# Performance work log

Measured on AMD Instinct MI355X. Metric: run time of the kernel, lower is better.

Reference implementation:

```python
import jax, jax.numpy as jnp
import numpy as np
from jax import lax

BETA = 0.5
IPOT_ITERS = 20


def cosine_cost(x, y):
    # x: [bs, n, D], y: [bs, m, D] -> 1 - cos_sim, [bs, n, m]
    x = x / (jnp.linalg.norm(x, axis=2, keepdims=True) + 1e-12)
    y = y / (jnp.linalg.norm(y, axis=2, keepdims=True) + 1e-12)
    return 1.0 - jnp.einsum('bnd,bmd->bnm', x, y)


def ipot_T(C, miu, nu, beta=BETA, iters=IPOT_ITERS):
    bs, n, m = C.shape
    A = jnp.exp(-C / beta)                    # [bs, n, m]
    sigma0 = jnp.ones((bs, m, 1), C.dtype) / m
    T0 = jnp.ones((bs, n, m), C.dtype)

    def step(carry, _):
        T, sigma = carry
        T = A * T
        delta = miu[:, :, None] / (T @ sigma + 1e-6)            # [bs, n, 1]
        sigma = nu[:, :, None] / (jnp.swapaxes(T, 1, 2) @ delta + 1e-6)  # [bs, m, 1]
        T = delta * T * jnp.swapaxes(sigma, 1, 2)
        return (T, sigma), None

    (T, _), _ = lax.scan(step, (T0, sigma0), None, length=iters)
    return lax.stop_gradient(T)  # original code detaches T


def ipot_distance(C):
    bs, n, m = C.shape
    miu = jnp.ones((bs, n), C.dtype) / n
    nu = jnp.ones((bs, m), C.dtype) / m
    T = ipot_T(C, miu, nu)
    return -jnp.sum(T * C, axis=(1, 2))  # note: original (un-exponentiated) C


def setup_inputs() -> dict:
    key = jax.random.key(0)
    k1, k2, k3, k4 = jax.random.split(key, 4)
    bs, n_sp, n_tm, D = 128, 196, 32, 768
    return {
        'spatial1': jax.random.normal(k1, (bs, n_sp, D), dtype=jnp.float32),
        'spatial2': jax.random.normal(k2, (bs, n_sp, D), dtype=jnp.float32),
        'temporal1': jax.random.normal(k3, (bs, n_tm, D), dtype=jnp.float32),
        'temporal2': jax.random.normal(k4, (bs, n_tm, D), dtype=jnp.float32),
    }


def reference(spatial1, spatial2, temporal1, temporal2):
    C_sp = cosine_cost(spatial1, spatial2)
    C_tm = cosine_cost(temporal1, temporal2)
    spatial_loss = ipot_distance(C_sp)
    temporal_loss = ipot_distance(C_tm)
    return spatial_loss.mean() + temporal_loss.mean()
```

## Files before the change

kernel.cpp:

```cpp
#include <hip/hip_runtime.h>
#include <hip/hip_bf16.h>
#include <cstdint>

typedef float f32x4 __attribute__((ext_vector_type(4)));
typedef __bf16 bf16x8 __attribute__((ext_vector_type(8)));

#define BS 128
#define NSP 196
#define NTM 32
#define DDIM 768

__device__ inline ushort4 f4_to_bf4(float4 v)
{
    ushort4 u;
    u.x = __builtin_bit_cast(unsigned short, (__bf16)v.x);
    u.y = __builtin_bit_cast(unsigned short, (__bf16)v.y);
    u.z = __builtin_bit_cast(unsigned short, (__bf16)v.z);
    u.w = __builtin_bit_cast(unsigned short, (__bf16)v.w);
    return u;
}

__device__ inline bf16x8 f4x2_to_bf8(float4 lo, float4 hi)
{
    bf16x8 r;
    r[0] = (__bf16)lo.x; r[1] = (__bf16)lo.y; r[2] = (__bf16)lo.z; r[3] = (__bf16)lo.w;
    r[4] = (__bf16)hi.x; r[5] = (__bf16)hi.y; r[6] = (__bf16)hi.z; r[7] = (__bf16)hi.w;
    return r;
}

__device__ inline float sumsq4(float4 a)
{
    return fmaf(a.x, a.x, fmaf(a.y, a.y, fmaf(a.z, a.z, a.w * a.w)));
}

__device__ inline float row16_sum(float x)
{
    int t;
    t = __builtin_amdgcn_update_dpp(0, __builtin_bit_cast(int, x), 0x121, 0xf, 0xf, true);
    x += __builtin_bit_cast(float, t);
    t = __builtin_amdgcn_update_dpp(0, __builtin_bit_cast(int, x), 0x122, 0xf, 0xf, true);
    x += __builtin_bit_cast(float, t);
    t = __builtin_amdgcn_update_dpp(0, __builtin_bit_cast(int, x), 0x124, 0xf, 0xf, true);
    x += __builtin_bit_cast(float, t);
    t = __builtin_amdgcn_update_dpp(0, __builtin_bit_cast(int, x), 0x128, 0xf, 0xf, true);
    x += __builtin_bit_cast(float, t);
    return x;
}

__global__ __launch_bounds__(256)
void tm_norm_kernel(const float* __restrict__ tm1, const float* __restrict__ tm2,
                    float* __restrict__ inx_tm, float* __restrict__ iny_tm)
{
    int B = blockIdx.x;
    const float* src; float* inv;
    if (B < 1024) { src = tm1; inv = inx_tm; }
    else          { B -= 1024; src = tm2; inv = iny_tm; }
    const int row  = B * 4 + (threadIdx.x >> 6);
    const int lane = threadIdx.x & 63;
    const float4* p = reinterpret_cast<const float4*>(src + (size_t)row * DDIM);
    float ss = 0.f;
#pragma unroll
    for (int c = 0; c < 3; ++c) ss += sumsq4(p[lane + 64 * c]);
#pragma unroll
    for (int off = 32; off; off >>= 1) ss += __shfl_xor(ss, off, 64);
    if (lane == 0) inv[row] = 1.0f / (sqrtf(ss) + 1e-12f);
}

__global__ __launch_bounds__(448)
void cost_gemm_sp2(const float* __restrict__ X, const float* __restrict__ Y,
                   __bf16* __restrict__ Aout)
{
    __shared__ __bf16 lds[11264];
    float* ldsF = reinterpret_cast<float*>(lds);

    const int flat  = blockIdx.x;
    const int xcd   = flat & 7;
    const int s     = flat >> 3;
    const int b     = xcd * 16 + (s >> 3);
    const int rem   = s & 7;
    const int r0    = (rem >> 2) * 112;
    const int ct_   = rem & 3;
    const int n0    = (ct_ < 3) ? ct_ * 64 : 132;

    const int tid  = threadIdx.x;
    const int w    = tid >> 6, lane = tid & 63;
    const int q    = lane >> 4, l16 = lane & 15;
    const int srow = tid >> 3;
    const int sslt = tid & 7;

    const float* Yb = Y + (size_t)b * NSP * DDIM;

    float4 aL[2], aH[2], bL, bH, b2L, b2H;
    float ssA[2] = {0.f, 0.f};
    float ssB = 0.f, ssB2 = 0.f;

    auto LOADS = [&](int k0) {
#pragma unroll
        for (int p = 0; p < 2; ++p) {
            int gr = b * NSP + r0 + srow + 56 * p;
            gr = min(gr, BS * NSP - 1);
            const float* sp = X + (size_t)gr * DDIM + k0 + sslt * 8;
            aL[p] = *reinterpret_cast<const float4*>(sp);
            aH[p] = *reinterpret_cast<const float4*>(sp + 4);
        }
        {
            const float* sp = Yb + (size_t)(n0 + srow) * DDIM + k0 + sslt * 8;
            bL = *reinterpret_cast<const float4*>(sp);
            bH = *reinterpret_cast<const float4*>(sp + 4);
        }
        if (tid < 64) {
            const float* sp = Yb + (size_t)(n0 + 56 + srow) * DDIM + k0 + sslt * 8;
            b2L = *reinterpret_cast<const float4*>(sp);
            b2H = *reinterpret_cast<const float4*>(sp + 4);
        }
    };
    auto WRITES = [&]() {
#pragma unroll
        for (int p = 0; p < 2; ++p) {
            int r = srow + 56 * p;
            ssA[p] += sumsq4(aL[p]) + sumsq4(aH[p]);
            *reinterpret_cast<bf16x8*>(&lds[r * 64 + ((sslt ^ (r & 7)) << 3)]) =
                f4x2_to_bf8(aL[p], aH[p]);
        }
        {
            int r = srow;
            ssB += sumsq4(bL) + sumsq4(bH);
            *reinterpret_cast<bf16x8*>(&lds[7168 + r * 64 + ((sslt ^ (r & 7)) << 3)]) =
                f4x2_to_bf8(bL, bH);
        }
        if (tid < 64) {
            int r = 56 + srow;
            ssB2 += sumsq4(b2L) + sumsq4(b2H);
            *reinterpret_cast<bf16x8*>(&lds[7168 + r * 64 + ((sslt ^ (r & 7)) << 3)]) =
                f4x2_to_bf8(b2L, b2H);
        }
    };

    f32x4 acc[4];
#pragma unroll
    for (int j = 0; j < 4; ++j) acc[j] = f32x4{0.f, 0.f, 0.f, 0.f};

    LOADS(0);
    for (int kt = 0; kt < 12; ++kt) {
        if (kt) __syncthreads();
        WRITES();
        __syncthreads();
        if (kt < 11) LOADS((kt + 1) * 64);
#pragma unroll
        for (int ks = 0; ks < 2; ++ks) {
            bf16x8 af, bf[4];
            {
                int r = w * 16 + l16;
                af = *reinterpret_cast<const bf16x8*>(
                    &lds[r * 64 + (((ks * 4 + q) ^ (r & 7)) << 3)]);
            }
#pragma unroll
            for (int ct = 0; ct < 4; ++ct) {
                int r = ct * 16 + l16;
                bf[ct] = *reinterpret_cast<const bf16x8*>(
                    &lds[7168 + r * 64 + (((ks * 4 + q) ^ (r & 7)) << 3)]);
            }
#pragma unroll
            for (int ct = 0; ct < 4; ++ct)
                acc[ct] = __builtin_amdgcn_mfma_f32_16x16x32_bf16(af, bf[ct], acc[ct], 0, 0, 0);
        }
    }
    __syncthreads();

#pragma unroll
    for (int p = 0; p < 2; ++p) ldsF[(srow + 56 * p) * 8 + sslt] = ssA[p];
    ldsF[896 + srow * 8 + sslt] = ssB;
    if (tid < 64) ldsF[896 + (56 + srow) * 8 + sslt] = ssB2;
    __syncthreads();

    float ivy[4];
#pragma unroll
    for (int ct = 0; ct < 4; ++ct) {
        int jr = ct * 16 + l16;
        f32x4 s0 = *reinterpret_cast<const f32x4*>(&ldsF[896 + jr * 8]);
        f32x4 s1 = *reinterpret_cast<const f32x4*>(&ldsF[896 + jr * 8 + 4]);
        float ss = (s0.x + s0.y) + (s0.z + s0.w) + (s1.x + s1.y) + (s1.z + s1.w);
        ivy[ct] = 1.0f / (sqrtf(ss) + 1e-12f);
    }
#pragma unroll
    for (int rr = 0; rr < 4; ++rr) {
        int i = w * 16 + q * 4 + rr;
        int gi = r0 + i;
        if (gi < NSP) {
            f32x4 s0 = *reinterpret_cast<const f32x4*>(&ldsF[i * 8]);
            f32x4 s1 = *reinterpret_cast<const f32x4*>(&ldsF[i * 8 + 4]);
            float ss = (s0.x + s0.y) + (s0.z + s0.w) + (s1.x + s1.y) + (s1.z + s1.w);
            float ivx = 1.0f / (sqrtf(ss) + 1e-12f);
#pragma unroll
            for (int ct = 0; ct < 4; ++ct) {
                float cs = acc[ct][rr] * ivx * ivy[ct];
                Aout[(size_t)b * 65536 + (size_t)gi * 256 + (n0 + ct * 16 + l16)] =
                    (__bf16)__expf(2.0f * cs - 2.0f);
            }
        }
    }
}

template<int WROWS, int NWAVES, int BN, int NPTS>
__global__ __launch_bounds__(NWAVES * 64)
void cost_gemm(const float* __restrict__ X, const float* __restrict__ Y,
               const float* __restrict__ invx, const float* __restrict__ invy,
               float* __restrict__ Aout)
{
    constexpr int MT = WROWS * NWAVES;
    constexpr int CT = BN / 16;
    constexpr int RT = WROWS / 16;
    constexpr int KP = 40;
    constexpr int NTH = NWAVES * 64;
    __shared__ __bf16 As[MT][KP];
    __shared__ __bf16 Bs[BN][KP];

    const int b    = blockIdx.y;
    const int row0 = blockIdx.x * MT;
    const int tid  = threadIdx.x;
    const int w    = tid >> 6, lane = tid & 63;
    const int q    = lane >> 4, l16 = lane & 15;
    const float* Xb = X + (size_t)b * NPTS * DDIM;
    const float* Yb = Y + (size_t)b * NPTS * DDIM;

    f32x4 acc[RT][CT];
#pragma unroll
    for (int i = 0; i < RT; ++i)
#pragma unroll
        for (int j = 0; j < CT; ++j) acc[i][j] = f32x4{0.f, 0.f, 0.f, 0.f};

    for (int k0 = 0; k0 < DDIM; k0 += 32) {
        __syncthreads();
        for (int idx = tid * 4; idx < MT * 32; idx += NTH * 4) {
            int r = idx >> 5, kk = idx & 31;
            int gr = row0 + r;
            float4 v = {0.f, 0.f, 0.f, 0.f};
            if (gr < NPTS) v = *reinterpret_cast<const float4*>(Xb + (size_t)gr * DDIM + k0 + kk);
            *reinterpret_cast<ushort4*>(&As[r][kk]) = f4_to_bf4(v);
        }
        for (int idx = tid * 4; idx < BN * 32; idx += NTH * 4) {
            int r = idx >> 5, kk = idx & 31;
            float4 v = {0.f, 0.f, 0.f, 0.f};
            if (r < NPTS) v = *reinterpret_cast<const float4*>(Yb + (size_t)r * DDIM + k0 + kk);
            *reinterpret_cast<ushort4*>(&Bs[r][kk]) = f4_to_bf4(v);
        }
        __syncthreads();

        bf16x8 af[RT];
#pragma unroll
        for (int rt = 0; rt < RT; ++rt)
            af[rt] = *reinterpret_cast<const bf16x8*>(&As[w * WROWS + rt * 16 + l16][q * 8]);
#pragma unroll
        for (int ct = 0; ct < CT; ++ct) {
            bf16x8 bfr = *reinterpret_cast<const bf16x8*>(&Bs[ct * 16 + l16][q * 8]);
#pragma unroll
            for (int rt = 0; rt < RT; ++rt)
                acc[rt][ct] = __builtin_amdgcn_mfma_f32_16x16x32_bf16(af[rt], bfr, acc[rt][ct], 0, 0, 0);
        }
    }

#pragma unroll
    for (int rt = 0; rt < RT; ++rt)
#pragma unroll
        for (int ct = 0; ct < CT; ++ct)
#pragma unroll
            for (int rr = 0; rr < 4; ++rr) {
                int i = row0 + w * WROWS + rt * 16 + q * 4 + rr;
                int j = ct * 16 + l16;
                if (i < NPTS && j < NPTS) {
                    float g  = acc[rt][ct][rr];
                    float cs = g * invx[b * NPTS + i] * invy[b * NPTS + j];
                    Aout[(size_t)b * NPTS * NPTS + (size_t)i * NPTS + j] = expf(-2.0f * (1.0f - cs));
                }
            }
}

__global__ __launch_bounds__(512, 1)
void ipot_dpp(const __bf16* __restrict__ Asp, const float* __restrict__ Atm,
              float* __restrict__ out)
{
    __shared__ __bf16 Alds[224 * 256];
    __shared__ float  cpart[32 * 260];
    __shared__ float  svec[2][272];
    __shared__ float  wsum[8];

    const int B = blockIdx.x;
    if (B >= 128) {
        if (threadIdx.x >= 64) return;
        const int b = B - 128;
        const float* Ab = Atm + (size_t)b * NTM * NTM;
        const int lane = threadIdx.x;
        const int rh = lane >> 5, cj = lane & 31;
        constexpr float MIU = 1.f / NTM;
        float A[16], P[16];
#pragma unroll
        for (int k = 0; k < 16; ++k) {
            A[k] = Ab[(rh + 2 * k) * NTM + cj];
            P[k] = 1.f;
        }
        float sv = MIU;
        for (int it = 0; it < 20; ++it) {
#pragma unroll
            for (int k = 0; k < 16; ++k) {
                P[k] *= A[k];
                float acc = row16_sum(P[k] * sv);
                acc += __shfl_xor(acc, 16);
                P[k] *= MIU * __builtin_amdgcn_rcpf(acc + 1e-6f);
            }
            float cssum = 0.f;
#pragma unroll
            for (int k = 0; k < 16; ++k) cssum += P[k];
            cssum += __shfl_xor(cssum, 32);
            float sg = MIU * __builtin_amdgcn_rcpf(cssum + 1e-6f);
#pragma unroll
            for (int k = 0; k < 16; ++k) P[k] *= sg;
            sv = sg;
        }
        float acc = 0.f;
#pragma unroll
        for (int k = 0; k < 16; ++k)
            acc = fmaf(P[k], -0.5f * __logf(A[k]), acc);
        acc = row16_sum(acc);
        acc += __shfl_xor(acc, 16);
        acc += __shfl_xor(acc, 32);
        if (lane == 0) atomicAdd(out, -acc * (1.f / BS));
        return;
    }

    const int b = (B & 7) * 16 + (B >> 3);
    const __bf16* Ab = Asp + (size_t)b * 65536;
    const int tid = threadIdx.x;
    const int w = tid >> 6, lane = tid & 63;
    const int rq = lane >> 4, cl = lane & 15;
    const int g = w * 4 + rq;
    const int colbase = cl * 8;
    constexpr float MIU = 1.f / NSP;

    for (int idx = tid; idx < NSP * 32; idx += 512) {
        int r = idx >> 5, c = idx & 31;
        bf16x8 v;
#pragma unroll
        for (int i = 0; i < 8; ++i) v[i] = (__bf16)0.f;
        if (c < 25) {
            v = *reinterpret_cast<const bf16x8*>(&Ab[(size_t)r * 256 + c * 8]);
            if (c == 24) { v[4] = (__bf16)0.f; v[5] = (__bf16)0.f; v[6] = (__bf16)0.f; v[7] = (__bf16)0.f; }
        }
        *reinterpret_cast<bf16x8*>(&Alds[r * 256 + c * 8]) = v;
    }
    {
        ushort4 z = {0, 0, 0, 0};
        for (int idx = tid; idx < 28 * 64; idx += 512) {
            int r = 196 + (idx >> 6), c4 = (idx & 63) << 2;
            *reinterpret_cast<ushort4*>(&Alds[r * 256 + c4]) = z;
        }
    }
    __syncthreads();

    float P[7][16];
#pragma unroll
    for (int k = 0; k < 7; ++k)
#pragma unroll
        for (int e = 0; e < 16; ++e) P[k][e] = 1.f;

    float sr[16];
#pragma unroll
    for (int e = 0; e < 16; ++e) {
        int j = (e < 8) ? (colbase + e) : (colbase + 128 + (e - 8));
        sr[e] = (j < NSP) ? MIU : 0.f;
    }

    for (int it = 0; it < 20; ++it) {
        float cs[16];
#pragma unroll
        for (int e = 0; e < 16; ++e) cs[e] = 0.f;

#pragma unroll
        for (int k = 0; k < 7; ++k) {
            const __bf16* ap = &Alds[(g + 32 * k) * 256 + colbase];
            bf16x8 a0 = *reinterpret_cast<const bf16x8*>(ap);
            bf16x8 a1 = *reinterpret_cast<const bf16x8*>(ap + 128);
            float r0 = 0.f, r1 = 0.f;
#pragma unroll
            for (int e = 0; e < 8; ++e) {
                P[k][e] *= (float)a0[e];
                r0 = fmaf(P[k][e], sr[e], r0);
            }
#pragma unroll
            for (int e = 0; e < 8; ++e) {
                P[k][8 + e] *= (float)a1[e];
                r1 = fmaf(P[k][8 + e], sr[8 + e], r1);
            }
            float racc = row16_sum(r0 + r1);
            float delta = MIU * __builtin_amdgcn_rcpf(racc + 1e-6f);
#pragma unroll
            for (int e = 0; e < 16; ++e) {
                P[k][e] *= delta;
                cs[e] += P[k][e];
            }
        }
        {
            float* cp = &cpart[g * 260 + colbase];
            *reinterpret_cast<f32x4*>(cp)     = f32x4{cs[0], cs[1], cs[2], cs[3]};
            *reinterpret_cast<f32x4*>(cp + 4) = f32x4{cs[4], cs[5], cs[6], cs[7]};
            float* cp2 = cp + 128;
            *reinterpret_cast<f32x4*>(cp2)     = f32x4{cs[8], cs[9], cs[10], cs[11]};
            *reinterpret_cast<f32x4*>(cp2 + 4) = f32x4{cs[12], cs[13], cs[14], cs[15]};
        }
        __syncthreads();
        if (tid < 256) {
            float s0 = 0.f, s1 = 0.f, s2 = 0.f, s3 = 0.f;
#pragma unroll
            for (int gg = 0; gg < 32; gg += 4) {
                s0 += cpart[(gg + 0) * 260 + tid];
                s1 += cpart[(gg + 1) * 260 + tid];
                s2 += cpart[(gg + 2) * 260 + tid];
                s3 += cpart[(gg + 3) * 260 + tid];
            }
            float sum = (s0 + s1) + (s2 + s3);
            svec[it & 1][tid] = (tid < NSP) ? (MIU * __builtin_amdgcn_rcpf(sum + 1e-6f)) : 0.f;
        }
        __syncthreads();
        {
            const float* sv = svec[it & 1];
            f32x4 t0 = *reinterpret_cast<const f32x4*>(&sv[colbase]);
            f32x4 t1 = *reinterpret_cast<const f32x4*>(&sv[colbase + 4]);
            f32x4 t2 = *reinterpret_cast<const f32x4*>(&sv[colbase + 128]);
            f32x4 t3 = *reinterpret_cast<const f32x4*>(&sv[colbase + 132]);
            sr[0] = t0.x; sr[1] = t0.y; sr[2] = t0.z; sr[3] = t0.w;
            sr[4] = t1.x; sr[5] = t1.y; sr[6] = t1.z; sr[7] = t1.w;
            sr[8] = t2.x; sr[9] = t2.y; sr[10] = t2.z; sr[11] = t2.w;
            sr[12] = t3.x; sr[13] = t3.y; sr[14] = t3.z; sr[15] = t3.w;
        }
#pragma unroll
        for (int k = 0; k < 7; ++k)
#pragma unroll
            for (int e = 0; e < 16; ++e) P[k][e] *= sr[e];
    }

    float acc = 0.f;
#pragma unroll
    for (int k = 0; k < 7; ++k) {
        const __bf16* ap = &Alds[(g + 32 * k) * 256 + colbase];
        bf16x8 a0 = *reinterpret_cast<const bf16x8*>(ap);
        bf16x8 a1 = *reinterpret_cast<const bf16x8*>(ap + 128);
#pragma unroll
        for (int e = 0; e < 8; ++e) {
            acc = fmaf(P[k][e],     -0.5f * __logf(fmaxf((float)a0[e], 1e-30f)), acc);
            acc = fmaf(P[k][8 + e], -0.5f * __logf(fmaxf((float)a1[e], 1e-30f)), acc);
        }
    }
    acc = row16_sum(acc);
    acc += __shfl_xor(acc, 16);
    acc += __shfl_xor(acc, 32);
    if (lane == 0) wsum[w] = acc;
    __syncthreads();
    if (tid == 0) {
        float t = 0.f;
#pragma unroll
        for (int i = 0; i < 8; ++i) t += wsum[i];
        atomicAdd(out, -t * (1.f / BS));
    }
}

extern "C" void kernel_launch(void* const* d_in, const int* in_sizes, int n_in,
                              void* d_out, int out_size, void* d_ws, size_t ws_size,
                              hipStream_t stream)
{
    const float* sp1 = (const float*)d_in[0];
    const float* sp2 = (const float*)d_in[1];
    const float* tm1 = (const float*)d_in[2];
    const float* tm2 = (const float*)d_in[3];
    float* out = (float*)d_out;
    float* ws  = (float*)d_ws;

    float* inx_tm = ws;
    float* iny_tm = inx_tm + BS * NTM;
    float* A_tm   = iny_tm + BS * NTM;
    __bf16* A_sp  = (__bf16*)(ws + 139264);

    tm_norm_kernel<<<dim3(2048), 256, 0, stream>>>(tm1, tm2, inx_tm, iny_tm);

    cost_gemm_sp2<<<dim3(1024), 448, 0, stream>>>(sp1, sp2, A_sp);

    cost_gemm<16, 2, 32, NTM><<<dim3(1, BS), 128, 0, stream>>>(tm1, tm2, inx_tm, iny_tm, A_tm);

    (void)hipMemsetAsync(d_out, 0, sizeof(float), stream);

    ipot_dpp<<<dim3(256), 512, 0, stream>>>(A_sp, A_tm, out);
}
```

Baseline: 147.0 us.

## Fuse spatial cost GEMM into IPOT kernel, keeping kernel matrix in LDS

Removes the separate spatial cost-GEMM kernel. Each IPOT block now computes its batch's full 196x196 cosine-similarity GEMM with MFMA, exponentiates it, and writes the kernel matrix directly into LDS, so the global bf16 round-trip and one launch go away. The column-sum reduction now does a cross-lane shuffle first, cutting the LDS partials from 32 groups to 8. The cost is that the GEMM work, about 3.9 GFLOP, is spread over only 128 blocks (one per CU) instead of 1024 blocks, with large accumulator register pressure, which can leave the GEMM underparallelized.

After: 166.7 us. +13.4%, slower.

```diff
diff --git a/kernel.cpp b/kernel.cpp
--- a/kernel.cpp
+++ b/kernel.cpp
@@ -66,141 +66,6 @@
     if (lane == 0) inv[row] = 1.0f / (sqrtf(ss) + 1e-12f);
 }
 
-__global__ __launch_bounds__(448)
-void cost_gemm_sp2(const float* __restrict__ X, const float* __restrict__ Y,
-                   __bf16* __restrict__ Aout)
-{
-    __shared__ __bf16 lds[11264];
-    float* ldsF = reinterpret_cast<float*>(lds);
-
-    const int flat  = blockIdx.x;
-    const int xcd   = flat & 7;
-    const int s     = flat >> 3;
-    const int b     = xcd * 16 + (s >> 3);
-    const int rem   = s & 7;
-    const int r0    = (rem >> 2) * 112;
-    const int ct_   = rem & 3;
-    const int n0    = (ct_ < 3) ? ct_ * 64 : 132;
-
-    const int tid  = threadIdx.x;
-    const int w    = tid >> 6, lane = tid & 63;
-    const int q    = lane >> 4, l16 = lane & 15;
-    const int srow = tid >> 3;
-    const int sslt = tid & 7;
-
-    const float* Yb = Y + (size_t)b * NSP * DDIM;
-
-    float4 aL[2], aH[2], bL, bH, b2L, b2H;
-    float ssA[2] = {0.f, 0.f};
-    float ssB = 0.f, ssB2 = 0.f;
-
-    auto LOADS = [&](int k0) {
-#pragma unroll
-        for (int p = 0; p < 2; ++p) {
-            int gr = b * NSP + r0 + srow + 56 * p;
-            gr = min(gr, BS * NSP - 1);
-            const float* sp = X + (size_t)gr * DDIM + k0 + sslt * 8;
-            aL[p] = *reinterpret_cast<const float4*>(sp);
-            aH[p] = *reinterpret_cast<const float4*>(sp + 4);
-        }
-        {
-            const float* sp = Yb + (size_t)(n0 + srow) * DDIM + k0 + sslt * 8;
-            bL = *reinterpret_cast<const float4*>(sp);
-            bH = *reinterpret_cast<const float4*>(sp + 4);
-        }
-        if (tid < 64) {
-            const float* sp = Yb + (size_t)(n0 + 56 + srow) * DDIM + k0 + sslt * 8;
-            b2L = *reinterpret_cast<const float4*>(sp);
-            b2H = *reinterpret_cast<const float4*>(sp + 4);
-        }
-    };
-    auto WRITES = [&]() {
-#pragma unroll
-        for (int p = 0; p < 2; ++p) {
-            int r = srow + 56 * p;
-            ssA[p] += sumsq4(aL[p]) + sumsq4(aH[p]);
-            *reinterpret_cast<bf16x8*>(&lds[r * 64 + ((sslt ^ (r & 7)) << 3)]) =
-                f4x2_to_bf8(aL[p], aH[p]);
-        }
-        {
-            int r = srow;
-            ssB += sumsq4(bL) + sumsq4(bH);
-            *reinterpret_cast<bf16x8*>(&lds[7168 + r * 64 + ((sslt ^ (r & 7)) << 3)]) =
-                f4x2_to_bf8(bL, bH);
-        }
-        if (tid < 64) {
-            int r = 56 + srow;
-            ssB2 += sumsq4(b2L) + sumsq4(b2H);
-            *reinterpret_cast<bf16x8*>(&lds[7168 + r * 64 + ((sslt ^ (r & 7)) << 3)]) =
-                f4x2_to_bf8(b2L, b2H);
-        }
-    };
-
-    f32x4 acc[4];
-#pragma unroll
-    for (int j = 0; j < 4; ++j) acc[j] = f32x4{0.f, 0.f, 0.f, 0.f};
-
-    LOADS(0);
-    for (int kt = 0; kt < 12; ++kt) {
-        if (kt) __syncthreads();
-        WRITES();
-        __syncthreads();
-        if (kt < 11) LOADS((kt + 1) * 64);
-#pragma unroll
-        for (int ks = 0; ks < 2; ++ks) {
-            bf16x8 af, bf[4];
-            {
-                int r = w * 16 + l16;
-                af = *reinterpret_cast<const bf16x8*>(
-                    &lds[r * 64 + (((ks * 4 + q) ^ (r & 7)) << 3)]);
-            }
-#pragma unroll
-            for (int ct = 0; ct < 4; ++ct) {
-                int r = ct * 16 + l16;
-                bf[ct] = *reinterpret_cast<const bf16x8*>(
-                    &lds[7168 + r * 64 + (((ks * 4 + q) ^ (r & 7)) << 3)]);
-            }
-#pragma unroll
-            for (int ct = 0; ct < 4; ++ct)
-                acc[ct] = __builtin_amdgcn_mfma_f32_16x16x32_bf16(af, bf[ct], acc[ct], 0, 0, 0);
-        }
-    }
-    __syncthreads();
-
-#pragma unroll
-    for (int p = 0; p < 2; ++p) ldsF[(srow + 56 * p) * 8 + sslt] = ssA[p];
-    ldsF[896 + srow * 8 + sslt] = ssB;
-    if (tid < 64) ldsF[896 + (56 + srow) * 8 + sslt] = ssB2;
-    __syncthreads();
-
-    float ivy[4];
-#pragma unroll
-    for (int ct = 0; ct < 4; ++ct) {
-        int jr = ct * 16 + l16;
-        f32x4 s0 = *reinterpret_cast<const f32x4*>(&ldsF[896 + jr * 8]);
-        f32x4 s1 = *reinterpret_cast<const f32x4*>(&ldsF[896 + jr * 8 + 4]);
-        float ss = (s0.x + s0.y) + (s0.z + s0.w) + (s1.x + s1.y) + (s1.z + s1.w);
-        ivy[ct] = 1.0f / (sqrtf(ss) + 1e-12f);
-    }
-#pragma unroll
-    for (int rr = 0; rr < 4; ++rr) {
-        int i = w * 16 + q * 4 + rr;
-        int gi = r0 + i;
-        if (gi < NSP) {
-            f32x4 s0 = *reinterpret_cast<const f32x4*>(&ldsF[i * 8]);
-            f32x4 s1 = *reinterpret_cast<const f32x4*>(&ldsF[i * 8 + 4]);
-            float ss = (s0.x + s0.y) + (s0.z + s0.w) + (s1.x + s1.y) + (s1.z + s1.w);
-            float ivx = 1.0f / (sqrtf(ss) + 1e-12f);
-#pragma unroll
-            for (int ct = 0; ct < 4; ++ct) {
-                float cs = acc[ct][rr] * ivx * ivy[ct];
-                Aout[(size_t)b * 65536 + (size_t)gi * 256 + (n0 + ct * 16 + l16)] =
-                    (__bf16)__expf(2.0f * cs - 2.0f);
-            }
-        }
-    }
-}
-
 template<int WROWS, int NWAVES, int BN, int NPTS>
 __global__ __launch_bounds__(NWAVES * 64)
 void cost_gemm(const float* __restrict__ X, const float* __restrict__ Y,
@@ -276,13 +141,11 @@
 }
 
 __global__ __launch_bounds__(512, 1)
-void ipot_dpp(const __bf16* __restrict__ Asp, const float* __restrict__ Atm,
-              float* __restrict__ out)
+void fused_sp(const float* __restrict__ X, const float* __restrict__ Y,
+              const float* __restrict__ Atm, float* __restrict__ out)
 {
     __shared__ __bf16 Alds[224 * 256];
-    __shared__ float  cpart[32 * 260];
-    __shared__ float  svec[2][272];
-    __shared__ float  wsum[8];
+    __shared__ __bf16 stage[15360];
 
     const int B = blockIdx.x;
     if (B >= 128) {
@@ -327,34 +190,129 @@
         return;
     }
 
-    const int b = (B & 7) * 16 + (B >> 3);
-    const __bf16* Ab = Asp + (size_t)b * 65536;
+    const int b = B;
     const int tid = threadIdx.x;
     const int w = tid >> 6, lane = tid & 63;
-    const int rq = lane >> 4, cl = lane & 15;
+    const int q = lane >> 4, l16 = lane & 15;
+    const bool p2 = (w < 6);
+
+    const int xr = tid >> 1;
+    const int h  = tid & 1;
+    const int gx = b * NSP + min(xr, NSP - 1);
+    const int gy = b * NSP + min(xr, NSP - 1);
+
+    float4 xv0, xv1, xv2, xv3, yv0, yv1, yv2, yv3;
+    float ssX = 0.f, ssY = 0.f;
+
+    auto LOADS = [&](int kt) {
+        int k0 = kt * 32 + h * 16;
+        if (tid < 448) {
+            const float* p = X + (size_t)gx * DDIM + k0;
+            xv0 = *reinterpret_cast<const float4*>(p);
+            xv1 = *reinterpret_cast<const float4*>(p + 4);
+            xv2 = *reinterpret_cast<const float4*>(p + 8);
+            xv3 = *reinterpret_cast<const float4*>(p + 12);
+        }
+        const float* py = Y + (size_t)gy * DDIM + k0;
+        yv0 = *reinterpret_cast<const float4*>(py);
+        yv1 = *reinterpret_cast<const float4*>(py + 4);
+        yv2 = *reinterpret_cast<const float4*>(py + 8);
+        yv3 = *reinterpret_cast<const float4*>(py + 12);
+    };
+    auto WRITES = [&]() {
+        if (tid < 448) {
+            ssX += sumsq4(xv0) + sumsq4(xv1) + sumsq4(xv2) + sumsq4(xv3);
+            int base = xr * 32;
+            int s0 = 2 * h, s1 = 2 * h + 1;
+            *reinterpret_cast<bf16x8*>(&stage[base + ((s0 ^ (xr & 3)) << 3)]) = f4x2_to_bf8(xv0, xv1);
+            *reinterpret_cast<bf16x8*>(&stage[base + ((s1 ^ (xr & 3)) << 3)]) = f4x2_to_bf8(xv2, xv3);
+        }
+        {
+            ssY += sumsq4(yv0) + sumsq4(yv1) + sumsq4(yv2) + sumsq4(yv3);
+            int base = 7168 + xr * 32;
+            int s0 = 2 * h, s1 = 2 * h + 1;
+            *reinterpret_cast<bf16x8*>(&stage[base + ((s0 ^ (xr & 3)) << 3)]) = f4x2_to_bf8(yv0, yv1);
+            *reinterpret_cast<bf16x8*>(&stage[base + ((s1 ^ (xr & 3)) << 3)]) = f4x2_to_bf8(yv2, yv3);
+        }
+    };
+
+    f32x4 acc0[16], acc1[16];
+#pragma unroll
+    for (int j = 0; j < 16; ++j) {
+        acc0[j] = f32x4{0.f, 0.f, 0.f, 0.f};
+        acc1[j] = f32x4{0.f, 0.f, 0.f, 0.f};
+    }
+
+    LOADS(0);
+    for (int kt = 0; kt < 24; ++kt) {
+        if (kt) __syncthreads();
+        WRITES();
+        __syncthreads();
+        if (kt < 23) LOADS(kt + 1);
+        int ra0 = w * 16 + l16;
+        bf16x8 af0 = *reinterpret_cast<const bf16x8*>(&stage[ra0 * 32 + ((q ^ (ra0 & 3)) << 3)]);
+        bf16x8 af1 = af0;
+        if (p2) {
+            int ra1 = (8 + w) * 16 + l16;
+            af1 = *reinterpret_cast<const bf16x8*>(&stage[ra1 * 32 + ((q ^ (ra1 & 3)) << 3)]);
+        }
+#pragma unroll
+        for (int ct = 0; ct < 16; ++ct) {
+            int rb = ct * 16 + l16;
+            bf16x8 bfr = *reinterpret_cast<const bf16x8*>(&stage[7168 + rb * 32 + ((q ^ (rb & 3)) << 3)]);
+            acc0[ct] = __builtin_amdgcn_mfma_f32_16x16x32_bf16(af0, bfr, acc0[ct], 0, 0, 0);
+            if (p2)
+                acc1[ct] = __builtin_amdgcn_mfma_f32_16x16x32_bf16(af1, bfr, acc1[ct], 0, 0, 0);
+        }
+    }
+    __syncthreads();
+
+    float* sF = reinterpret_cast<float*>(stage);
+    if (tid < 448) sF[tid] = ssX;
+    sF[512 + tid] = ssY;
+    __syncthreads();
+
+    float ivy[16];
+#pragma unroll
+    for (int ct = 0; ct < 16; ++ct) {
+        int j = ct * 16 + l16;
+        ivy[ct] = 1.0f / (sqrtf(sF[512 + 2 * j] + sF[513 + 2 * j]) + 1e-12f);
+    }
+#pragma unroll
+    for (int rr = 0; rr < 4; ++rr) {
+        int i = w * 16 + q * 4 + rr;
+        float ivx = 1.0f / (sqrtf(sF[2 * i] + sF[2 * i + 1]) + 1e-12f);
+#pragma unroll
+        for (int ct = 0; ct < 16; ++ct) {
+            int j = ct * 16 + l16;
+            float a = (i < NSP && j < NSP) ? __expf(2.0f * acc0[ct][rr] * ivx * ivy[ct] - 2.0f) : 0.f;
+            Alds[i * 256 + j] = (__bf16)a;
+        }
+    }
+    if (p2) {
+#pragma unroll
+        for (int rr = 0; rr < 4; ++rr) {
+            int i = (8 + w) * 16 + q * 4 + rr;
+            float ivx = 1.0f / (sqrtf(sF[2 * i] + sF[2 * i + 1]) + 1e-12f);
+#pragma unroll
+            for (int ct = 0; ct < 16; ++ct) {
+                int j = ct * 16 + l16;
+                float a = (i < NSP && j < NSP) ? __expf(2.0f * acc1[ct][rr] * ivx * ivy[ct] - 2.0f) : 0.f;
+                Alds[i * 256 + j] = (__bf16)a;
+            }
+        }
+    }
+    __syncthreads();
+
+    float* cpart = sF;
+    float* svec  = sF + 2080;
+    float* wsum  = sF + 2624;
+
+    const int rq = q;
+    const int cl = l16;
     const int g = w * 4 + rq;
     const int colbase = cl * 8;
     constexpr float MIU = 1.f / NSP;
-
-    for (int idx = tid; idx < NSP * 32; idx += 512) {
-        int r = idx >> 5, c = idx & 31;
-        bf16x8 v;
-#pragma unroll
-        for (int i = 0; i < 8; ++i) v[i] = (__bf16)0.f;
-        if (c < 25) {
-            v = *reinterpret_cast<const bf16x8*>(&Ab[(size_t)r * 256 + c * 8]);
-            if (c == 24) { v[4] = (__bf16)0.f; v[5] = (__bf16)0.f; v[6] = (__bf16)0.f; v[7] = (__bf16)0.f; }
-        }
-        *reinterpret_cast<bf16x8*>(&Alds[r * 256 + c * 8]) = v;
-    }
-    {
-        ushort4 z = {0, 0, 0, 0};
-        for (int idx = tid; idx < 28 * 64; idx += 512) {
-            int r = 196 + (idx >> 6), c4 = (idx & 63) << 2;
-            *reinterpret_cast<ushort4*>(&Alds[r * 256 + c4]) = z;
-        }
-    }
-    __syncthreads();
 
     float P[7][16];
 #pragma unroll
@@ -398,8 +356,13 @@
                 cs[e] += P[k][e];
             }
         }
-        {
-            float* cp = &cpart[g * 260 + colbase];
+#pragma unroll
+        for (int e = 0; e < 16; ++e) {
+            cs[e] += __shfl_xor(cs[e], 16);
+            cs[e] += __shfl_xor(cs[e], 32);
+        }
+        if (rq == 0) {
+            float* cp = &cpart[w * 260 + colbase];
             *reinterpret_cast<f32x4*>(cp)     = f32x4{cs[0], cs[1], cs[2], cs[3]};
             *reinterpret_cast<f32x4*>(cp + 4) = f32x4{cs[4], cs[5], cs[6], cs[7]};
             float* cp2 = cp + 128;
@@ -408,20 +371,18 @@
         }
         __syncthreads();
         if (tid < 256) {
-            float s0 = 0.f, s1 = 0.f, s2 = 0.f, s3 = 0.f;
-#pragma unroll
-            for (int gg = 0; gg < 32; gg += 4) {
+            float s0 = 0.f, s1 = 0.f;
+#pragma unroll
+            for (int gg = 0; gg < 8; gg += 2) {
                 s0 += cpart[(gg + 0) * 260 + tid];
                 s1 += cpart[(gg + 1) * 260 + tid];
-                s2 += cpart[(gg + 2) * 260 + tid];
-                s3 += cpart[(gg + 3) * 260 + tid];
-            }
-            float sum = (s0 + s1) + (s2 + s3);
-            svec[it & 1][tid] = (tid < NSP) ? (MIU * __builtin_amdgcn_rcpf(sum + 1e-6f)) : 0.f;
+            }
+            float sum = s0 + s1;
+            svec[(it & 1) * 272 + tid] = (tid < NSP) ? (MIU * __builtin_amdgcn_rcpf(sum + 1e-6f)) : 0.f;
         }
         __syncthreads();
         {
-            const float* sv = svec[it & 1];
+            const float* sv = svec + (it & 1) * 272;
             f32x4 t0 = *reinterpret_cast<const f32x4*>(&sv[colbase]);
             f32x4 t1 = *reinterpret_cast<const f32x4*>(&sv[colbase + 4]);
             f32x4 t2 = *reinterpret_cast<const f32x4*>(&sv[colbase + 128]);
@@ -476,15 +437,12 @@
     float* inx_tm = ws;
     float* iny_tm = inx_tm + BS * NTM;
     float* A_tm   = iny_tm + BS * NTM;
-    __bf16* A_sp  = (__bf16*)(ws + 139264);
 
     tm_norm_kernel<<<dim3(2048), 256, 0, stream>>>(tm1, tm2, inx_tm, iny_tm);
 
-    cost_gemm_sp2<<<dim3(1024), 448, 0, stream>>>(sp1, sp2, A_sp);
-
     cost_gemm<16, 2, 32, NTM><<<dim3(1, BS), 128, 0, stream>>>(tm1, tm2, inx_tm, iny_tm, A_tm);
 
     (void)hipMemsetAsync(d_out, 0, sizeof(float), stream);
 
-    ipot_dpp<<<dim3(256), 512, 0, stream>>>(A_sp, A_tm, out);
-}
+    fused_sp<<<dim3(256), 512, 0, stream>>>(sp1, sp2, A_tm, out);
+}
```

## Double-buffer LDS and register prefetch two K-tiles ahead in spatial cost GEMM

Applied to the files above, without the earlier changes.

Splits the spatial cost GEMM's shared-memory tile into two buffers and keeps two sets of prefetch registers, so global loads run two K-tiles ahead. Each phase writes one buffer, syncs once, issues the next load, then runs MFMAs. This drops one of the two barriers per K-step and gives the global loads more time in flight. The cost is double the LDS (about 45KB) and more registers, which may lower occupancy.

Measured after the change: 169.4 us. 15.2% more time.

```diff
diff --git a/kernel.cpp b/kernel.cpp
--- a/kernel.cpp
+++ b/kernel.cpp
@@ -67,10 +67,10 @@
 }
 
 __global__ __launch_bounds__(448)
-void cost_gemm_sp2(const float* __restrict__ X, const float* __restrict__ Y,
+void cost_gemm_sp4(const float* __restrict__ X, const float* __restrict__ Y,
                    __bf16* __restrict__ Aout)
 {
-    __shared__ __bf16 lds[11264];
+    __shared__ __bf16 lds[22528];
     float* ldsF = reinterpret_cast<float*>(lds);
 
     const int flat  = blockIdx.x;
@@ -90,11 +90,13 @@
 
     const float* Yb = Y + (size_t)b * NSP * DDIM;
 
-    float4 aL[2], aH[2], bL, bH, b2L, b2H;
+    float4 AL0[2], AH0[2], BL0, BH0, C2L0, C2H0;
+    float4 AL1[2], AH1[2], BL1, BH1, C2L1, C2H1;
     float ssA[2] = {0.f, 0.f};
     float ssB = 0.f, ssB2 = 0.f;
 
-    auto LOADS = [&](int k0) {
+    auto LOADS = [&](float4 (&aL)[2], float4 (&aH)[2], float4& bL, float4& bH,
+                     float4& b2L, float4& b2H, int k0) {
 #pragma unroll
         for (int p = 0; p < 2; ++p) {
             int gr = b * NSP + r0 + srow + 56 * p;
@@ -114,24 +116,25 @@
             b2H = *reinterpret_cast<const float4*>(sp + 4);
         }
     };
-    auto WRITES = [&]() {
+    auto WRITES = [&](int bb, float4 (&aL)[2], float4 (&aH)[2], float4& bL, float4& bH,
+                      float4& b2L, float4& b2H) {
 #pragma unroll
         for (int p = 0; p < 2; ++p) {
             int r = srow + 56 * p;
             ssA[p] += sumsq4(aL[p]) + sumsq4(aH[p]);
-            *reinterpret_cast<bf16x8*>(&lds[r * 64 + ((sslt ^ (r & 7)) << 3)]) =
+            *reinterpret_cast<bf16x8*>(&lds[bb + r * 64 + ((sslt ^ (r & 7)) << 3)]) =
                 f4x2_to_bf8(aL[p], aH[p]);
         }
         {
             int r = srow;
             ssB += sumsq4(bL) + sumsq4(bH);
-            *reinterpret_cast<bf16x8*>(&lds[7168 + r * 64 + ((sslt ^ (r & 7)) << 3)]) =
+            *reinterpret_cast<bf16x8*>(&lds[bb + 7168 + r * 64 + ((sslt ^ (r & 7)) << 3)]) =
                 f4x2_to_bf8(bL, bH);
         }
         if (tid < 64) {
             int r = 56 + srow;
             ssB2 += sumsq4(b2L) + sumsq4(b2H);
-            *reinterpret_cast<bf16x8*>(&lds[7168 + r * 64 + ((sslt ^ (r & 7)) << 3)]) =
+            *reinterpret_cast<bf16x8*>(&lds[bb + 7168 + r * 64 + ((sslt ^ (r & 7)) << 3)]) =
                 f4x2_to_bf8(b2L, b2H);
         }
     };
@@ -140,32 +143,52 @@
 #pragma unroll
     for (int j = 0; j < 4; ++j) acc[j] = f32x4{0.f, 0.f, 0.f, 0.f};
 
-    LOADS(0);
-    for (int kt = 0; kt < 12; ++kt) {
-        if (kt) __syncthreads();
-        WRITES();
-        __syncthreads();
-        if (kt < 11) LOADS((kt + 1) * 64);
+    auto MFMA = [&](int bb) {
 #pragma unroll
         for (int ks = 0; ks < 2; ++ks) {
             bf16x8 af, bf[4];
             {
                 int r = w * 16 + l16;
                 af = *reinterpret_cast<const bf16x8*>(
-                    &lds[r * 64 + (((ks * 4 + q) ^ (r & 7)) << 3)]);
+                    &lds[bb + r * 64 + (((ks * 4 + q) ^ (r & 7)) << 3)]);
             }
 #pragma unroll
             for (int ct = 0; ct < 4; ++ct) {
                 int r = ct * 16 + l16;
                 bf[ct] = *reinterpret_cast<const bf16x8*>(
-                    &lds[7168 + r * 64 + (((ks * 4 + q) ^ (r & 7)) << 3)]);
+                    &lds[bb + 7168 + r * 64 + (((ks * 4 + q) ^ (r & 7)) << 3)]);
             }
 #pragma unroll
             for (int ct = 0; ct < 4; ++ct)
                 acc[ct] = __builtin_amdgcn_mfma_f32_16x16x32_bf16(af, bf[ct], acc[ct], 0, 0, 0);
         }
-    }
+    };
+
+#define PHASE_SYNC()                                          \
+    asm volatile("s_waitcnt lgkmcnt(0)" ::: "memory");        \
+    __builtin_amdgcn_s_barrier();                             \
+    __builtin_amdgcn_sched_barrier(0);
+
+    LOADS(AL0, AH0, BL0, BH0, C2L0, C2H0, 0);
+    LOADS(AL1, AH1, BL1, BH1, C2L1, C2H1, 64);
+    for (int i = 0; i < 5; ++i) {
+        WRITES(0, AL0, AH0, BL0, BH0, C2L0, C2H0);
+        PHASE_SYNC();
+        LOADS(AL0, AH0, BL0, BH0, C2L0, C2H0, (2 * i + 2) * 64);
+        MFMA(0);
+        WRITES(11264, AL1, AH1, BL1, BH1, C2L1, C2H1);
+        PHASE_SYNC();
+        LOADS(AL1, AH1, BL1, BH1, C2L1, C2H1, (2 * i + 3) * 64);
+        MFMA(11264);
+    }
+    WRITES(0, AL0, AH0, BL0, BH0, C2L0, C2H0);
+    PHASE_SYNC();
+    MFMA(0);
+    WRITES(11264, AL1, AH1, BL1, BH1, C2L1, C2H1);
+    PHASE_SYNC();
+    MFMA(11264);
     __syncthreads();
+#undef PHASE_SYNC
 
 #pragma unroll
     for (int p = 0; p < 2; ++p) ldsF[(srow + 56 * p) * 8 + sslt] = ssA[p];
@@ -480,7 +503,7 @@
 
     tm_norm_kernel<<<dim3(2048), 256, 0, stream>>>(tm1, tm2, inx_tm, iny_tm);
 
-    cost_gemm_sp2<<<dim3(1024), 448, 0, stream>>>(sp1, sp2, A_sp);
+    cost_gemm_sp4<<<dim3(1024), 448, 0, stream>>>(sp1, sp2, A_sp);
 
     cost_gemm<16, 2, 32, NTM><<<dim3(1, BS), 128, 0, stream>>>(tm1, tm2, inx_tm, iny_tm, A_tm);
 
```

## Pre-convert spatial inputs to bf16 with norms, use bf16-input cost GEMM

Applied to the files above, without the earlier changes.

A new prep kernel computes inverse norms for both the spatial and temporal inputs, and in the same pass writes bf16 copies of the spatial inputs into workspace. A new cost GEMM reads those bf16 copies through double-buffered, XOR-swizzled LDS. Each block covers all 196 rows for one column tile, so the grid is 512 blocks instead of 1024. Normalization is applied in the epilogue instead of before the GEMM. This is meant to halve GEMM-side global reads and remove the normalization and conversion from the GEMM blocks, at the cost of an extra write and read of the bf16 copies and a larger workspace requirement. The old path stays as a fallback when the workspace is too small.

Result: slower. 165.1 us (+12.3%).

```diff
diff --git a/kernel.cpp b/kernel.cpp
--- a/kernel.cpp
+++ b/kernel.cpp
@@ -48,22 +48,162 @@
 }
 
 __global__ __launch_bounds__(256)
-void tm_norm_kernel(const float* __restrict__ tm1, const float* __restrict__ tm2,
-                    float* __restrict__ inx_tm, float* __restrict__ iny_tm)
+void prep2_kernel(const float* __restrict__ sp1, const float* __restrict__ sp2,
+                  const float* __restrict__ tm1, const float* __restrict__ tm2,
+                  float* __restrict__ inx_sp, float* __restrict__ iny_sp,
+                  float* __restrict__ inx_tm, float* __restrict__ iny_tm,
+                  __bf16* __restrict__ X16, __bf16* __restrict__ Y16)
 {
     int B = blockIdx.x;
-    const float* src; float* inv;
-    if (B < 1024) { src = tm1; inv = inx_tm; }
-    else          { B -= 1024; src = tm2; inv = iny_tm; }
-    const int row  = B * 4 + (threadIdx.x >> 6);
-    const int lane = threadIdx.x & 63;
-    const float4* p = reinterpret_cast<const float4*>(src + (size_t)row * DDIM);
-    float ss = 0.f;
-#pragma unroll
-    for (int c = 0; c < 3; ++c) ss += sumsq4(p[lane + 64 * c]);
-#pragma unroll
-    for (int off = 32; off; off >>= 1) ss += __shfl_xor(ss, off, 64);
-    if (lane == 0) inv[row] = 1.0f / (sqrtf(ss) + 1e-12f);
+    const float* src; float* inv; __bf16* dst;
+    if (B < 3136)      {            src = sp1; inv = inx_sp; dst = X16; }
+    else if (B < 6272) { B -= 3136; src = sp2; inv = iny_sp; dst = Y16; }
+    else if (B < 6784) { B -= 6272; src = tm1; inv = inx_tm; dst = nullptr; }
+    else               { B -= 6784; src = tm2; inv = iny_tm; dst = nullptr; }
+
+    const int wv = threadIdx.x >> 6, lane = threadIdx.x & 63;
+    const int r0 = B * 8 + wv * 2;
+    const int r1 = r0 + 1;
+    const float4* p0 = reinterpret_cast<const float4*>(src + (size_t)r0 * DDIM);
+    const float4* p1 = reinterpret_cast<const float4*>(src + (size_t)r1 * DDIM);
+
+    float4 v0[3], v1[3];
+#pragma unroll
+    for (int c = 0; c < 3; ++c) {
+        v0[c] = p0[lane + 64 * c];
+        v1[c] = p1[lane + 64 * c];
+    }
+    float s0 = 0.f, s1 = 0.f;
+#pragma unroll
+    for (int c = 0; c < 3; ++c) {
+        s0 += sumsq4(v0[c]);
+        s1 += sumsq4(v1[c]);
+    }
+#pragma unroll
+    for (int off = 32; off; off >>= 1) {
+        s0 += __shfl_xor(s0, off, 64);
+        s1 += __shfl_xor(s1, off, 64);
+    }
+    if (lane == 0) {
+        inv[r0] = 1.0f / (sqrtf(s0) + 1e-12f);
+        inv[r1] = 1.0f / (sqrtf(s1) + 1e-12f);
+    }
+    if (dst) {
+#pragma unroll
+        for (int c = 0; c < 3; ++c) {
+            *reinterpret_cast<ushort4*>(&dst[(size_t)r0 * DDIM + lane * 4 + 256 * c]) = f4_to_bf4(v0[c]);
+            *reinterpret_cast<ushort4*>(&dst[(size_t)r1 * DDIM + lane * 4 + 256 * c]) = f4_to_bf4(v1[c]);
+        }
+    }
+}
+
+#define GA_LDS 18432
+__global__ __launch_bounds__(448)
+void cost_gemm_sp16(const __bf16* __restrict__ X, const __bf16* __restrict__ Y,
+                    const float* __restrict__ invx, const float* __restrict__ invy,
+                    __bf16* __restrict__ Aout)
+{
+    __shared__ __bf16 lds[2 * GA_LDS];
+
+    const int flat  = blockIdx.x;
+    const int xcd   = flat & 7;
+    const int s     = flat >> 3;
+    const int b     = xcd * 16 + (s >> 2);
+    const int ctile = s & 3;
+    const int n0    = (ctile < 3) ? ctile * 64 : 132;
+
+    const int tid  = threadIdx.x;
+    const int w    = tid >> 6, lane = tid & 63;
+    const int q    = lane >> 4, l16 = lane & 15;
+    const int srow = tid >> 3;
+    const int sslt = tid & 7;
+
+    const __bf16* Yb = Y + (size_t)b * NSP * DDIM;
+
+    bf16x8 aR[4], bR, b2R;
+
+    auto LOADS = [&](int k0) {
+#pragma unroll
+        for (int p = 0; p < 4; ++p) {
+            int gr = b * NSP + srow + 56 * p;
+            gr = min(gr, BS * NSP - 1);
+            aR[p] = *reinterpret_cast<const bf16x8*>(X + (size_t)gr * DDIM + k0 + sslt * 8);
+        }
+        bR = *reinterpret_cast<const bf16x8*>(Yb + (size_t)(n0 + srow) * DDIM + k0 + sslt * 8);
+        if (tid < 64)
+            b2R = *reinterpret_cast<const bf16x8*>(Yb + (size_t)(n0 + 56 + srow) * DDIM + k0 + sslt * 8);
+    };
+    auto WRITES = [&](int buf) {
+#pragma unroll
+        for (int p = 0; p < 4; ++p) {
+            int r = srow + 56 * p;
+            *reinterpret_cast<bf16x8*>(&lds[buf * GA_LDS + r * 64 + ((sslt ^ (r & 7)) << 3)]) = aR[p];
+        }
+        {
+            int r = srow;
+            *reinterpret_cast<bf16x8*>(&lds[buf * GA_LDS + 14336 + r * 64 + ((sslt ^ (r & 7)) << 3)]) = bR;
+        }
+        if (tid < 64) {
+            int r = 56 + srow;
+            *reinterpret_cast<bf16x8*>(&lds[buf * GA_LDS + 14336 + r * 64 + ((sslt ^ (r & 7)) << 3)]) = b2R;
+        }
+    };
+
+    f32x4 acc[2][4];
+#pragma unroll
+    for (int i = 0; i < 2; ++i)
+#pragma unroll
+        for (int j = 0; j < 4; ++j) acc[i][j] = f32x4{0.f, 0.f, 0.f, 0.f};
+
+    LOADS(0);
+    int buf = 0;
+    for (int kt = 0; kt < 12; ++kt) {
+        WRITES(buf);
+        if (kt < 11) LOADS((kt + 1) * 64);
+        __syncthreads();
+#pragma unroll
+        for (int ks = 0; ks < 2; ++ks) {
+            bf16x8 af[2], bf[4];
+#pragma unroll
+            for (int rt = 0; rt < 2; ++rt) {
+                int r = w * 32 + rt * 16 + l16;
+                af[rt] = *reinterpret_cast<const bf16x8*>(
+                    &lds[buf * GA_LDS + r * 64 + (((ks * 4 + q) ^ (r & 7)) << 3)]);
+            }
+#pragma unroll
+            for (int ct = 0; ct < 4; ++ct) {
+                int r = ct * 16 + l16;
+                bf[ct] = *reinterpret_cast<const bf16x8*>(
+                    &lds[buf * GA_LDS + 14336 + r * 64 + (((ks * 4 + q) ^ (r & 7)) << 3)]);
+            }
+#pragma unroll
+            for (int ct = 0; ct < 4; ++ct)
+#pragma unroll
+                for (int rt = 0; rt < 2; ++rt)
+                    acc[rt][ct] = __builtin_amdgcn_mfma_f32_16x16x32_bf16(af[rt], bf[ct], acc[rt][ct], 0, 0, 0);
+        }
+        __syncthreads();
+        buf ^= 1;
+    }
+
+    float ivy[4];
+#pragma unroll
+    for (int ct = 0; ct < 4; ++ct) ivy[ct] = invy[b * NSP + n0 + ct * 16 + l16];
+#pragma unroll
+    for (int rt = 0; rt < 2; ++rt)
+#pragma unroll
+        for (int rr = 0; rr < 4; ++rr) {
+            int i = w * 32 + rt * 16 + q * 4 + rr;
+            if (i < NSP) {
+                float ivx = invx[b * NSP + i];
+#pragma unroll
+                for (int ct = 0; ct < 4; ++ct) {
+                    int j = n0 + ct * 16 + l16;
+                    float cs = acc[rt][ct][rr] * ivx * ivy[ct];
+                    Aout[(size_t)b * 65536 + (size_t)i * 256 + j] = (__bf16)__expf(2.0f * cs - 2.0f);
+                }
+            }
+        }
 }
 
 __global__ __launch_bounds__(448)
@@ -473,14 +613,26 @@
     float* out = (float*)d_out;
     float* ws  = (float*)d_ws;
 
-    float* inx_tm = ws;
+    float* inx_sp = ws;
+    float* iny_sp = inx_sp + BS * NSP;
+    float* inx_tm = iny_sp + BS * NSP;
     float* iny_tm = inx_tm + BS * NTM;
     float* A_tm   = iny_tm + BS * NTM;
-    __bf16* A_sp  = (__bf16*)(ws + 139264);
-
-    tm_norm_kernel<<<dim3(2048), 256, 0, stream>>>(tm1, tm2, inx_tm, iny_tm);
-
-    cost_gemm_sp2<<<dim3(1024), 448, 0, stream>>>(sp1, sp2, A_sp);
+    __bf16* A_sp  = (__bf16*)(ws + 189440);
+    char*   base  = (char*)d_ws;
+    __bf16* X16   = (__bf16*)(base + 34312192);
+    __bf16* Y16   = (__bf16*)(base + 72847360);
+    const size_t NEED = 111382528;
+    const bool fast = (ws_size >= NEED);
+
+    prep2_kernel<<<dim3(7296), 256, 0, stream>>>(sp1, sp2, tm1, tm2,
+                                                 inx_sp, iny_sp, inx_tm, iny_tm,
+                                                 fast ? X16 : nullptr, fast ? Y16 : nullptr);
+
+    if (fast)
+        cost_gemm_sp16<<<dim3(512), 448, 0, stream>>>(X16, Y16, inx_sp, iny_sp, A_sp);
+    else
+        cost_gemm_sp2<<<dim3(1024), 448, 0, stream>>>(sp1, sp2, A_sp);
 
     cost_gemm<16, 2, 32, NTM><<<dim3(1, BS), 128, 0, stream>>>(tm1, tm2, inx_tm, iny_tm, A_tm);
 
```
